# Kernel optimization log

Measured on AMD Instinct MI355X. Metric: run time of the kernel, lower is better.

The kernel has to match this reference:

```python
import jax, jax.numpy as jnp
import numpy as np

HEADS = 16
DIM_HEAD = 64
CHUNK = 64
EPS_LN = 1e-5
EPS_T5 = 1e-6


def _layernorm(x, g, b):
    mu = x.mean(-1, keepdims=True)
    var = x.var(-1, keepdims=True)
    return (x - mu) / jnp.sqrt(var + EPS_LN) * g + b


def _t5norm(x, w):
    # T5LayerNorm variant: divide by (||x|| * d^-0.5), i.e. RMS norm
    norm = jnp.linalg.norm(x, axis=-1, keepdims=True) * (x.shape[-1] ** -0.5)
    return x / jnp.maximum(norm, EPS_T5) * w


def _rotary(t, freqs):
    rot = freqs.shape[-1]
    t1, t2 = t[..., :rot], t[..., rot:]
    half = rot // 2
    a, b = t1[..., :half], t1[..., half:]
    rh = jnp.concatenate((-b, a), axis=-1)  # rotate_half
    t1 = t1 * jnp.cos(freqs) + rh * jnp.sin(freqs)
    return jnp.concatenate((t1, t2), axis=-1)


def _split_heads(t):
    B, N, _ = t.shape
    return t.reshape(B, N, HEADS, DIM_HEAD).transpose(0, 2, 1, 3)


def _merge_heads(t):
    B, H, N, D = t.shape
    return t.transpose(0, 2, 1, 3).reshape(B, N, H * D)


def _attend(q, k, v, causal=False):
    sim = jnp.einsum('bhid,bhjd->bhij', q, k)
    if causal:
        i, j = sim.shape[-2:]
        m = jnp.triu(jnp.ones((i, j), bool), j - i + 1)
        sim = jnp.where(m, jnp.finfo(sim.dtype).min, sim)
    attn = jax.nn.softmax(sim, axis=-1)
    return jnp.einsum('bhij,bhjd->bhid', attn, v)


def setup_inputs() -> dict:
    key = jax.random.key(0)
    ks = jax.random.split(key, 20)
    b, n, d = 4, 1024, 1024
    kc, r, rn = n // CHUNK, 2, 2 * CHUNK
    dff = 4 * d
    s = 0.02

    def W(i, *shape):
        return jax.random.normal(ks[i], shape, jnp.float32) * s

    return {
        'hidden_states': jax.random.normal(ks[0], (b, n, d), jnp.float32),
        'retrieval': jax.random.normal(ks[1], (b, kc, r, rn, d), jnp.float32),
        'q_pos_emb': jax.random.normal(ks[2], (1, 1, CHUNK, DIM_HEAD), jnp.float32),
        'k_pos_emb': jax.random.normal(ks[3], (1, 1, rn, DIM_HEAD), jnp.float32),
        'ln1_g': jnp.ones(d), 'ln1_b': jnp.zeros(d),
        'Wq_s': W(4, d, d), 'Wk_s': W(5, d, d), 'Wv_s': W(6, d, d),
        'Wo_s': W(7, d, d), 'bo_s': jnp.zeros(d),
        'ln2_g': jnp.ones(d), 'ln2_b': jnp.zeros(d),
        'Wq_c': W(8, d, d), 'Wk_c': W(9, d, d), 'Wv_c': W(10, d, d),
        'Wo_c': W(11, d, d), 'bo_c': jnp.zeros(d),
        'null_k': jax.random.normal(ks[12], (d,), jnp.float32),
        'null_v': jax.random.normal(ks[13], (d,), jnp.float32),
        'post_w': jnp.ones(d),
        'W1': W(14, d, dff), 'b1': jnp.zeros(dff),
        'W2': W(15, dff, d), 'b2': jnp.zeros(d),
    }


def reference(hidden_states, retrieval, q_pos_emb, k_pos_emb,
              ln1_g, ln1_b, Wq_s, Wk_s, Wv_s, Wo_s, bo_s,
              ln2_g, ln2_b, Wq_c, Wk_c, Wv_c, Wo_c, bo_c,
              null_k, null_v, post_w, W1, b1, W2, b2):
    b, n, d = hidden_states.shape
    scale = DIM_HEAD ** -0.5

    # --- causal self-attention (pre-LN) ---
    x = _layernorm(hidden_states, ln1_g, ln1_b)
    q = _split_heads(x @ Wq_s) * scale
    k = _split_heads(x @ Wk_s)
    v = _split_heads(x @ Wv_s)
    o = _merge_heads(_attend(q, k, v, causal=True)) @ Wo_s + bo_s
    hs = _layernorm(o + hidden_states, ln2_g, ln2_b)
    residual = hs  # residual taken after ln_2, before cross-attn (per source)

    # --- chunked cross-attention over retrieved neighbor chunks ---
    kc, r, rn = retrieval.shape[1:4]
    cp = CHUNK - 1  # causal padding
    seq_index = (n // CHUNK) * CHUNK
    # shift queries back by chunk_size-1 (causality), pad tail with zeros
    xq = jnp.pad(hs[:, cp:], ((0, 0), (0, cp), (0, 0)))[:, :seq_index]
    xq = xq.reshape(b * kc, CHUNK, d)
    ctx = retrieval.reshape(b * kc, r * rn, d)
    qpe = jnp.pad(q_pos_emb[:, :, cp:], ((0, 0), (0, 0), (0, cp), (0, 0)))
    kpe = jnp.tile(k_pos_emb, (1, 1, r, 1))  # 'b h n d -> b h (r n) d'
    q = _rotary(_split_heads(xq @ Wq_c) * scale, qpe)
    kk = _rotary(_split_heads(ctx @ Wk_c), kpe)
    vv = _split_heads(ctx @ Wv_c)
    nk = jnp.broadcast_to(null_k.reshape(1, HEADS, 1, DIM_HEAD), (b * kc, HEADS, 1, DIM_HEAD))
    nv = jnp.broadcast_to(null_v.reshape(1, HEADS, 1, DIM_HEAD), (b * kc, HEADS, 1, DIM_HEAD))
    kk = jnp.concatenate((nk, kk), axis=2)
    vv = jnp.concatenate((nv, vv), axis=2)
    cca = _merge_heads(_attend(q, kk, vv)) @ Wo_c + bo_c
    cca = cca.reshape(b, seq_index, d)
    # shift output forward by chunk_size-1, crop to n
    cca = jnp.pad(cca, ((0, 0), (cp, 0), (0, 0)))[:, :n]
    # PostNorm wrapper: T5 norm of (fn(x) + x)
    hs = _t5norm(cca + hs, post_w)

    # --- GPTNeo MLP (gelu-new / tanh approx) ---
    ff = jax.nn.gelu(hs @ W1 + b1, approximate=True) @ W2 + b2
    return residual + ff
```

## Files before the change

kernel.cpp:

```cpp
#include <hip/hip_runtime.h>
#include <hip/hip_bf16.h>
#include <math.h>

using u16 = unsigned short;

static constexpr int SEQ = 1024;
static constexpr int DM  = 1024;
static constexpr int DHD = 64;

typedef __bf16 bfv8 __attribute__((ext_vector_type(8)));
typedef float  f32x4 __attribute__((ext_vector_type(4)));

__device__ __forceinline__ float u2f(u16 u) {
  return __uint_as_float(((unsigned int)u) << 16);
}
__device__ __forceinline__ u16 f2b(float x) {
  __hip_bfloat16 h = __float2bfloat16(x);
  return *reinterpret_cast<u16*>(&h);
}
__device__ __forceinline__ void gload16(const u16* g, u16* l) {
  __builtin_amdgcn_global_load_lds(
      (const __attribute__((address_space(1))) unsigned int*)g,
      (__attribute__((address_space(3))) unsigned int*)l, 16, 0, 0);
}

template <int OT , bool HASBIAS, bool HASRES, bool DOGELU, bool ROT, int DBUF>
__global__ __launch_bounds__(256) void mgemm_k(
    const u16* __restrict__ A, const u16* __restrict__ Bt, void* __restrict__ C,
    int M, int K, int ldc, int coff, float alpha0, float alpha1, int acol,
    const float* __restrict__ bias, const float* __restrict__ res,
    const float* __restrict__ tab) {
  constexpr int NBUF = DBUF ? 2 : 1;
  __shared__ u16 As[NBUF][128 * 64];
  __shared__ u16 Bs[NBUF][128 * 64];
  const int tid = threadIdx.x;
  const int w = tid >> 6, lane = tid & 63;
  const int wr = w >> 1, wc = w & 1;

  const int nwg = gridDim.x * gridDim.y;
  const int bid = blockIdx.y * gridDim.x + blockIdx.x;
  const int qq = nwg >> 3, r8 = nwg & 7;
  const int xcd = bid & 7, pos = bid >> 3;
  const int cbase = (xcd < r8) ? xcd * (qq + 1) : r8 * (qq + 1) + (xcd - r8) * qq;
  const int logical = cbase + pos;
  const int row0 = (logical / gridDim.x) << 7;
  const int col0 = (logical % gridDim.x) << 7;

  f32x4 acc[4][4] = {};

  auto STAGE = [&](int buf, int k0) {
#pragma unroll
    for (int i = 0; i < 4; ++i) {
      const int c = ((w << 2) + i) * 64 + lane;
      const int r = c >> 3;
      const int cbs = ((c & 7) ^ (r & 7)) << 3;
      const int r64 = r & 63;
      const int rB = (r & 64) | ((r64 & 15) << 2) | (r64 >> 4);
      gload16(A + (size_t)(row0 + r) * K + k0 + cbs, &As[buf][((w << 2) + i) << 9]);
      gload16(Bt + (size_t)(col0 + rB) * K + k0 + cbs, &Bs[buf][((w << 2) + i) << 9]);
    }
  };
  auto COMPUTE = [&](int buf) {
#pragma unroll
    for (int kk = 0; kk < 2; ++kk) {
      bfv8 af[4], bfr[4];
#pragma unroll
      for (int m = 0; m < 4; ++m) {
        const int ar = (wr << 6) + (m << 4) + (lane & 15);
        const int sl = ((kk << 2) | (lane >> 4)) ^ (ar & 7);
        af[m] = *reinterpret_cast<const bfv8*>(&As[buf][ar * 64 + (sl << 3)]);
      }
#pragma unroll
      for (int n = 0; n < 4; ++n) {
        const int br = (wc << 6) + (n << 4) + (lane & 15);
        const int sl = ((kk << 2) | (lane >> 4)) ^ (br & 7);
        bfr[n] = *reinterpret_cast<const bfv8*>(&Bs[buf][br * 64 + (sl << 3)]);
      }
#pragma unroll
      for (int m = 0; m < 4; ++m)
#pragma unroll
        for (int n = 0; n < 4; ++n)
          acc[m][n] = __builtin_amdgcn_mfma_f32_16x16x32_bf16(af[m], bfr[n], acc[m][n], 0, 0, 0);
    }
  };

  if constexpr (DBUF) {
    STAGE(0, 0);
    int cur = 0;
    for (int k0 = 0; k0 < K; k0 += 64) {
      if (k0 + 64 < K) {
        STAGE(cur ^ 1, k0 + 64);
        asm volatile("s_waitcnt vmcnt(8)" ::: "memory");
      } else {
        asm volatile("s_waitcnt vmcnt(0)" ::: "memory");
      }
      __builtin_amdgcn_s_barrier();
      __builtin_amdgcn_sched_barrier(0);
      COMPUTE(cur);
      __builtin_amdgcn_s_barrier();
      cur ^= 1;
    }
  } else {
    for (int k0 = 0; k0 < K; k0 += 64) {
      STAGE(0, k0);
      __syncthreads();
      COMPUTE(0);
      __syncthreads();
    }
  }

  const int lr = (lane >> 4) << 2;
  const int lc = lane & 15;
  const int gcb = col0 + (wc << 6) + (lc << 2);
#pragma unroll
  for (int m = 0; m < 4; ++m) {
#pragma unroll
    for (int r = 0; r < 4; ++r) {
      const int gr = row0 + (wr << 6) + (m << 4) + lr + r;
      float t[4];
#pragma unroll
      for (int n = 0; n < 4; ++n)
        t[n] = acc[m][n][r] * ((gcb + n) < acol ? alpha0 : alpha1);
      if constexpr (ROT) {
        const int j = gr & 127;
        const int cc = gcb & 63;
        float4 c4 = *reinterpret_cast<const float4*>(tab + j * 64 + cc);
        float4 s4 = *reinterpret_cast<const float4*>(tab + 8192 + j * 64 + cc);
        const float cs[4] = {c4.x, c4.y, c4.z, c4.w};
        const float sn[4] = {s4.x, s4.y, s4.z, s4.w};
        float o2[4];
#pragma unroll
        for (int n = 0; n < 4; ++n) {
          const float pv = __shfl_xor(t[n], 8);
          const float part = (cc < 32) ? -pv : pv;
          o2[n] = t[n] * cs[n] + part * sn[n];
        }
#pragma unroll
        for (int n = 0; n < 4; ++n) t[n] = o2[n];
      }
      if constexpr (HASBIAS) {
        float4 b4 = *reinterpret_cast<const float4*>(bias + gcb);
        t[0] += b4.x; t[1] += b4.y; t[2] += b4.z; t[3] += b4.w;
      }
      if constexpr (DOGELU) {
#pragma unroll
        for (int n = 0; n < 4; ++n) {
          const float x = t[n];
          t[n] = 0.5f * x * (1.f + tanhf(0.7978845608f * (x + 0.044715f * x * x * x)));
        }
      }
      const size_t cb = (size_t)gr * ldc + coff + gcb;
      if constexpr (HASRES) {
        float4 r4 = *reinterpret_cast<const float4*>(res + cb);
        t[0] += r4.x; t[1] += r4.y; t[2] += r4.z; t[3] += r4.w;
      }
      if constexpr (OT == 0) {
        float4 o4 = make_float4(t[0], t[1], t[2], t[3]);
        *reinterpret_cast<float4*>((float*)C + cb) = o4;
      } else {
        ushort4 o4 = {f2b(t[0]), f2b(t[1]), f2b(t[2]), f2b(t[3])};
        *reinterpret_cast<ushort4*>((u16*)C + cb) = o4;
      }
    }
  }
}

__global__ __launch_bounds__(256) void costab_k(const float* __restrict__ kpe,
                                                float* __restrict__ tab) {
  const int i = blockIdx.x * 256 + threadIdx.x;
  const float f = kpe[i];
  tab[i] = cosf(f);
  tab[8192 + i] = sinf(f);
}

__global__ __launch_bounds__(256) void wtrans_k(const float* __restrict__ in,
                                                u16* __restrict__ out, int K, int N) {
  __shared__ float t[32][33];
  const int tx = threadIdx.x & 31, ty = threadIdx.x >> 5;
  const int r0 = blockIdx.y << 5, c0 = blockIdx.x << 5;
#pragma unroll
  for (int i = 0; i < 4; ++i)
    t[ty + 8 * i][tx] = in[(size_t)(r0 + ty + 8 * i) * N + c0 + tx];
  __syncthreads();
#pragma unroll
  for (int i = 0; i < 4; ++i)
    out[(size_t)(c0 + ty + 8 * i) * K + r0 + tx] = f2b(t[tx][ty + 8 * i]);
}

__global__ __launch_bounds__(256) void cast_k(const float* __restrict__ in,
                                              u16* __restrict__ out) {
  const int i = blockIdx.x * 256 + threadIdx.x;
  float4 v = reinterpret_cast<const float4*>(in)[i];
  ushort4 o = {f2b(v.x), f2b(v.y), f2b(v.z), f2b(v.w)};
  reinterpret_cast<ushort4*>(out)[i] = o;
}

__global__ __launch_bounds__(256) void ln_k(const float* __restrict__ in,
                                            const float* __restrict__ g,
                                            const float* __restrict__ b,
                                            u16* __restrict__ out) {
  const int tid = threadIdx.x;
  const int c = tid << 2;
  const size_t base = (size_t)blockIdx.x * DM;
  float4 x = *reinterpret_cast<const float4*>(in + base + c);
  float s = x.x + x.y + x.z + x.w;
  float ss = x.x * x.x + x.y * x.y + x.z * x.z + x.w * x.w;
#pragma unroll
  for (int m = 1; m < 64; m <<= 1) {
    s += __shfl_xor(s, m, 64);
    ss += __shfl_xor(ss, m, 64);
  }
  __shared__ float ls[4], lss[4];
  if ((tid & 63) == 0) { ls[tid >> 6] = s; lss[tid >> 6] = ss; }
  __syncthreads();
  s = (ls[0] + ls[1]) + (ls[2] + ls[3]);
  ss = (lss[0] + lss[1]) + (lss[2] + lss[3]);
  const float mu = s * (1.f / DM);
  const float var = ss * (1.f / DM) - mu * mu;
  const float rstd = rsqrtf(var + 1e-5f);
  float4 g4 = *reinterpret_cast<const float4*>(g + c);
  float4 b4 = *reinterpret_cast<const float4*>(b + c);
  ushort4 u;
  u.x = f2b((x.x - mu) * rstd * g4.x + b4.x);
  u.y = f2b((x.y - mu) * rstd * g4.y + b4.y);
  u.z = f2b((x.z - mu) * rstd * g4.z + b4.z);
  u.w = f2b((x.w - mu) * rstd * g4.w + b4.w);
  *reinterpret_cast<ushort4*>(out + base + c) = u;
}

__global__ __launch_bounds__(256) void ln2x_k(const float* __restrict__ in,
                                              const float* __restrict__ g,
                                              const float* __restrict__ b,
                                              float* __restrict__ hs,
                                              u16* __restrict__ xq) {
  const int tid = threadIdx.x;
  const int c = tid << 2;
  const int row = blockIdx.x;
  const size_t base = (size_t)row * DM;
  float4 x = *reinterpret_cast<const float4*>(in + base + c);
  float s = x.x + x.y + x.z + x.w;
  float ss = x.x * x.x + x.y * x.y + x.z * x.z + x.w * x.w;
#pragma unroll
  for (int m = 1; m < 64; m <<= 1) {
    s += __shfl_xor(s, m, 64);
    ss += __shfl_xor(ss, m, 64);
  }
  __shared__ float ls[4], lss[4];
  if ((tid & 63) == 0) { ls[tid >> 6] = s; lss[tid >> 6] = ss; }
  __syncthreads();
  s = (ls[0] + ls[1]) + (ls[2] + ls[3]);
  ss = (lss[0] + lss[1]) + (lss[2] + lss[3]);
  const float mu = s * (1.f / DM);
  const float var = ss * (1.f / DM) - mu * mu;
  const float rstd = rsqrtf(var + 1e-5f);
  float4 g4 = *reinterpret_cast<const float4*>(g + c);
  float4 b4 = *reinterpret_cast<const float4*>(b + c);
  float4 o;
  o.x = (x.x - mu) * rstd * g4.x + b4.x;
  o.y = (x.y - mu) * rstd * g4.y + b4.y;
  o.z = (x.z - mu) * rstd * g4.z + b4.z;
  o.w = (x.w - mu) * rstd * g4.w + b4.w;
  *reinterpret_cast<float4*>(hs + base + c) = o;
  const int local = row & (SEQ - 1);
  const int bb = row >> 10;
  if (local >= 63) {
    ushort4 u = {f2b(o.x), f2b(o.y), f2b(o.z), f2b(o.w)};
    *reinterpret_cast<ushort4*>(xq + (size_t)((bb << 10) + local - 63) * DM + c) = u;
  } else {
    ushort4 z = {0, 0, 0, 0};
    *reinterpret_cast<ushort4*>(xq + (size_t)((bb << 10) + 961 + local) * DM + c) = z;
  }
}

__global__ __launch_bounds__(256) void t5_k(const u16* __restrict__ cca,
                                            const float* __restrict__ hs,
                                            const float* __restrict__ w,
                                            u16* __restrict__ out) {
  const int tid = threadIdx.x;
  const int row = blockIdx.x;
  const int t = row & (SEQ - 1);
  const int c = tid << 2;
  const size_t base = (size_t)row * DM;
  float4 x = *reinterpret_cast<const float4*>(hs + base + c);
  if (t >= 63) {
    ushort4 cu = *reinterpret_cast<const ushort4*>(cca + base - (size_t)63 * DM + c);
    x.x += u2f(cu.x); x.y += u2f(cu.y); x.z += u2f(cu.z); x.w += u2f(cu.w);
  }
  float ss = x.x * x.x + x.y * x.y + x.z * x.z + x.w * x.w;
#pragma unroll
  for (int m = 1; m < 64; m <<= 1) ss += __shfl_xor(ss, m, 64);
  __shared__ float lss[4];
  if ((tid & 63) == 0) lss[tid >> 6] = ss;
  __syncthreads();
  ss = (lss[0] + lss[1]) + (lss[2] + lss[3]);
  const float rms = sqrtf(ss * (1.f / DM));
  const float inv = 1.f / fmaxf(rms, 1e-6f);
  float4 w4 = *reinterpret_cast<const float4*>(w + c);
  ushort4 o = {f2b(x.x * inv * w4.x), f2b(x.y * inv * w4.y),
               f2b(x.z * inv * w4.z), f2b(x.w * inv * w4.w)};
  *reinterpret_cast<ushort4*>(out + base + c) = o;
}

__global__ __launch_bounds__(256) void rotq_k(u16* __restrict__ q,
                                              const float* __restrict__ qpe) {
  __shared__ float rb[DM];
  const size_t base = (size_t)blockIdx.x * 64 * DM;
  const int e = threadIdx.x << 2;
  ushort4 u = *reinterpret_cast<const ushort4*>(q + base + e);
  rb[e + 0] = u2f(u.x); rb[e + 1] = u2f(u.y); rb[e + 2] = u2f(u.z); rb[e + 3] = u2f(u.w);
  __syncthreads();
  u16 ov[4];
#pragma unroll
  for (int k = 0; k < 4; ++k) {
    const int ee = e + k;
    const int cc = ee & 63;
    const float f = qpe[63 * 64 + cc];
    const float t1 = rb[ee];
    const float part = (cc < 32) ? -rb[ee + 32] : rb[ee - 32];
    ov[k] = f2b(t1 * cosf(f) + part * sinf(f));
  }
  ushort4 o = {ov[0], ov[1], ov[2], ov[3]};
  *reinterpret_cast<ushort4*>(q + base + e) = o;
}

__device__ __forceinline__ int vswz(int d, int k) {
  return (k & 7) | (((k >> 3) ^ ((d >> 2) & 7)) << 3);
}

__global__ __launch_bounds__(256) void attn_self_k(const u16* __restrict__ qkv,
                                                   u16* __restrict__ o) {
  const int qt = blockIdx.x, h = blockIdx.y, b = blockIdx.z;
  __shared__ u16 qs[64][72];
  __shared__ u16 ks[64][72];
  __shared__ u16 vt[64][72];
  __shared__ u16 ps[64][72];
  const int tid = threadIdx.x;
  const int w = tid >> 6, lane = tid & 63;
  const int strip = w << 4;
  const int lrow = lane & 15, lk = lane >> 4;
  const int rowb = b * SEQ;
  const int hoff = h * DHD;

#pragma unroll
  for (int rp = 0; rp < 4; ++rp) {
    const int fi = tid + (rp << 8);
    const int r = fi >> 4, c4 = (fi & 15) << 2;
    *reinterpret_cast<ushort4*>(&qs[r][c4]) =
        *reinterpret_cast<const ushort4*>(qkv + (size_t)(rowb + qt * 64 + r) * 3072 + hoff + c4);
  }

  ushort4 kr[4], vr[4];
  auto loadKV = [&](int kt) {
#pragma unroll
    for (int rp = 0; rp < 4; ++rp) {
      const int fi = tid + (rp << 8);
      const int r = fi >> 4, c4 = (fi & 15) << 2;
      const size_t g = (size_t)(rowb + kt * 64 + r) * 3072 + hoff + c4;
      kr[rp] = *reinterpret_cast<const ushort4*>(qkv + g + 1024);
      vr[rp] = *reinterpret_cast<const ushort4*>(qkv + g + 2048);
    }
  };
  loadKV(0);

  float mrun[4], lrun[4];
  f32x4 accO[4] = {};
#pragma unroll
  for (int r = 0; r < 4; ++r) { mrun[r] = -1e30f; lrun[r] = 0.f; }

  for (int kt = 0; kt <= qt; ++kt) {
    __syncthreads();
#pragma unroll
    for (int rp = 0; rp < 4; ++rp) {
      const int fi = tid + (rp << 8);
      const int r = fi >> 4, c4 = (fi & 15) << 2;
      *reinterpret_cast<ushort4*>(&ks[r][c4]) = kr[rp];
      vt[c4 + 0][vswz(c4 + 0, r)] = vr[rp].x;
      vt[c4 + 1][vswz(c4 + 1, r)] = vr[rp].y;
      vt[c4 + 2][vswz(c4 + 2, r)] = vr[rp].z;
      vt[c4 + 3][vswz(c4 + 3, r)] = vr[rp].w;
    }
    __syncthreads();
    if (kt < qt) loadKV(kt + 1);

    f32x4 sacc[4] = {};
#pragma unroll
    for (int kk = 0; kk < 2; ++kk) {
      bfv8 qf = *reinterpret_cast<const bfv8*>(&qs[strip + lrow][(kk << 5) + (lk << 3)]);
#pragma unroll
      for (int n = 0; n < 4; ++n) {
        bfv8 kf = *reinterpret_cast<const bfv8*>(&ks[(n << 4) + lrow][(kk << 5) + (lk << 3)]);
        sacc[n] = __builtin_amdgcn_mfma_f32_16x16x32_bf16(qf, kf, sacc[n], 0, 0, 0);
      }
    }
    if (kt == qt) {
#pragma unroll
      for (int n = 0; n < 4; ++n)
#pragma unroll
        for (int r = 0; r < 4; ++r)
          if ((n << 4) + lrow > strip + (lk << 2) + r) sacc[n][r] = -1e30f;
    }
#pragma unroll
    for (int r = 0; r < 4; ++r) {
      float mt = fmaxf(fmaxf(sacc[0][r], sacc[1][r]), fmaxf(sacc[2][r], sacc[3][r]));
      mt = fmaxf(mt, __shfl_xor(mt, 1));
      mt = fmaxf(mt, __shfl_xor(mt, 2));
      mt = fmaxf(mt, __shfl_xor(mt, 4));
      mt = fmaxf(mt, __shfl_xor(mt, 8));
      const float nm = fmaxf(mrun[r], mt);
      const float f = __expf(mrun[r] - nm);
      mrun[r] = nm;
      float p0 = __expf(sacc[0][r] - nm);
      float p1 = __expf(sacc[1][r] - nm);
      float p2 = __expf(sacc[2][r] - nm);
      float p3 = __expf(sacc[3][r] - nm);
      float rs = (p0 + p1) + (p2 + p3);
      rs += __shfl_xor(rs, 1);
      rs += __shfl_xor(rs, 2);
      rs += __shfl_xor(rs, 4);
      rs += __shfl_xor(rs, 8);
      lrun[r] = lrun[r] * f + rs;
#pragma unroll
      for (int nd = 0; nd < 4; ++nd) accO[nd][r] *= f;
      const int prow = strip + (lk << 2) + r;
      ps[prow][lrow +  0] = f2b(p0);
      ps[prow][lrow + 16] = f2b(p1);
      ps[prow][lrow + 32] = f2b(p2);
      ps[prow][lrow + 48] = f2b(p3);
    }
#pragma unroll
    for (int kk = 0; kk < 2; ++kk) {
      bfv8 pf = *reinterpret_cast<const bfv8*>(&ps[strip + lrow][(kk << 5) + (lk << 3)]);
#pragma unroll
      for (int nd = 0; nd < 4; ++nd) {
        const int vd = (nd << 4) + lrow;
        const int slot = ((kk << 2) | lk) ^ ((vd >> 2) & 7);
        bfv8 vf = *reinterpret_cast<const bfv8*>(&vt[vd][slot << 3]);
        accO[nd] = __builtin_amdgcn_mfma_f32_16x16x32_bf16(pf, vf, accO[nd], 0, 0, 0);
      }
    }
  }
#pragma unroll
  for (int r = 0; r < 4; ++r) {
    const float inv = 1.f / lrun[r];
    const size_t rowoff = (size_t)(rowb + qt * 64 + strip + (lk << 2) + r) * DM + hoff;
#pragma unroll
    for (int nd = 0; nd < 4; ++nd)
      o[rowoff + (nd << 4) + lrow] = f2b(accO[nd][r] * inv);
  }
}

__global__ __launch_bounds__(256) void attn_cca_k(
    const u16* __restrict__ q, const u16* __restrict__ kv,
    const float* __restrict__ nullk, const float* __restrict__ nullv,
    u16* __restrict__ o) {
  const int h = blockIdx.y, bk = blockIdx.z;
  __shared__ u16 qs[64][72];
  __shared__ u16 ks[64][72];
  __shared__ u16 vt[64][72];
  __shared__ u16 ps[64][72];
  const int tid = threadIdx.x;
  const int w = tid >> 6, lane = tid & 63;
  const int strip = w << 4;
  const int lrow = lane & 15, lk = lane >> 4;
  const int hoff = h * DHD;
  const size_t qbase = (size_t)bk * 64 * DM + hoff;

#pragma unroll
  for (int rp = 0; rp < 4; ++rp) {
    const int fi = tid + (rp << 8);
    const int r = fi >> 4, c4 = (fi & 15) << 2;
    *reinterpret_cast<ushort4*>(&qs[r][c4]) =
        *reinterpret_cast<const ushort4*>(q + qbase + (size_t)r * DM + c4);
  }

  ushort4 kr[4], vr[4];
  auto loadKV = [&](int kt) {
#pragma unroll
    for (int rp = 0; rp < 4; ++rp) {
      const int fi = tid + (rp << 8);
      const int r = fi >> 4, c4 = (fi & 15) << 2;
      const int kj = kt * 64 + r;
      ushort4 ku = {0, 0, 0, 0}, vu = {0, 0, 0, 0};
      if (kj == 0) {
        float4 nk4 = *reinterpret_cast<const float4*>(nullk + hoff + c4);
        float4 nv4 = *reinterpret_cast<const float4*>(nullv + hoff + c4);
        ku = {f2b(nk4.x), f2b(nk4.y), f2b(nk4.z), f2b(nk4.w)};
        vu = {f2b(nv4.x), f2b(nv4.y), f2b(nv4.z), f2b(nv4.w)};
      } else if (kj <= 256) {
        const size_t g = (size_t)(bk * 256 + kj - 1) * 2048 + hoff + c4;
        ku = *reinterpret_cast<const ushort4*>(kv + g);
        vu = *reinterpret_cast<const ushort4*>(kv + g + 1024);
      }
      kr[rp] = ku; vr[rp] = vu;
    }
  };
  loadKV(0);

  float mrun[4], lrun[4];
  f32x4 accO[4] = {};
#pragma unroll
  for (int r = 0; r < 4; ++r) { mrun[r] = -1e30f; lrun[r] = 0.f; }

  for (int kt = 0; kt < 5; ++kt) {
    __syncthreads();
#pragma unroll
    for (int rp = 0; rp < 4; ++rp) {
      const int fi = tid + (rp << 8);
      const int r = fi >> 4, c4 = (fi & 15) << 2;
      *reinterpret_cast<ushort4*>(&ks[r][c4]) = kr[rp];
      vt[c4 + 0][vswz(c4 + 0, r)] = vr[rp].x;
      vt[c4 + 1][vswz(c4 + 1, r)] = vr[rp].y;
      vt[c4 + 2][vswz(c4 + 2, r)] = vr[rp].z;
      vt[c4 + 3][vswz(c4 + 3, r)] = vr[rp].w;
    }
    __syncthreads();
    if (kt < 4) loadKV(kt + 1);

    f32x4 sacc[4] = {};
#pragma unroll
    for (int kk = 0; kk < 2; ++kk) {
      bfv8 qf = *reinterpret_cast<const bfv8*>(&qs[strip + lrow][(kk << 5) + (lk << 3)]);
#pragma unroll
      for (int n = 0; n < 4; ++n) {
        bfv8 kf = *reinterpret_cast<const bfv8*>(&ks[(n << 4) + lrow][(kk << 5) + (lk << 3)]);
        sacc[n] = __builtin_amdgcn_mfma_f32_16x16x32_bf16(qf, kf, sacc[n], 0, 0, 0);
      }
    }
    if (kt == 4) {
#pragma unroll
      for (int n = 0; n < 4; ++n)
#pragma unroll
        for (int r = 0; r < 4; ++r)
          if ((n << 4) + lrow >= 1) sacc[n][r] = -1e30f;
    }
#pragma unroll
    for (int r = 0; r < 4; ++r) {
      float mt = fmaxf(fmaxf(sacc[0][r], sacc[1][r]), fmaxf(sacc[2][r], sacc[3][r]));
      mt = fmaxf(mt, __shfl_xor(mt, 1));
      mt = fmaxf(mt, __shfl_xor(mt, 2));
      mt = fmaxf(mt, __shfl_xor(mt, 4));
      mt = fmaxf(mt, __shfl_xor(mt, 8));
      const float nm = fmaxf(mrun[r], mt);
      const float f = __expf(mrun[r] - nm);
      mrun[r] = nm;
      float p0 = __expf(sacc[0][r] - nm);
      float p1 = __expf(sacc[1][r] - nm);
      float p2 = __expf(sacc[2][r] - nm);
      float p3 = __expf(sacc[3][r] - nm);
      float rs = (p0 + p1) + (p2 + p3);
      rs += __shfl_xor(rs, 1);
      rs += __shfl_xor(rs, 2);
      rs += __shfl_xor(rs, 4);
      rs += __shfl_xor(rs, 8);
      lrun[r] = lrun[r] * f + rs;
#pragma unroll
      for (int nd = 0; nd < 4; ++nd) accO[nd][r] *= f;
      const int prow = strip + (lk << 2) + r;
      ps[prow][lrow +  0] = f2b(p0);
      ps[prow][lrow + 16] = f2b(p1);
      ps[prow][lrow + 32] = f2b(p2);
      ps[prow][lrow + 48] = f2b(p3);
    }
#pragma unroll
    for (int kk = 0; kk < 2; ++kk) {
      bfv8 pf = *reinterpret_cast<const bfv8*>(&ps[strip + lrow][(kk << 5) + (lk << 3)]);
#pragma unroll
      for (int nd = 0; nd < 4; ++nd) {
        const int vd = (nd << 4) + lrow;
        const int slot = ((kk << 2) | lk) ^ ((vd >> 2) & 7);
        bfv8 vf = *reinterpret_cast<const bfv8*>(&vt[vd][slot << 3]);
        accO[nd] = __builtin_amdgcn_mfma_f32_16x16x32_bf16(pf, vf, accO[nd], 0, 0, 0);
      }
    }
  }
#pragma unroll
  for (int r = 0; r < 4; ++r) {
    const float inv = 1.f / lrun[r];
    const size_t rowoff = (size_t)(bk * 64 + strip + (lk << 2) + r) * DM + hoff;
#pragma unroll
    for (int nd = 0; nd < 4; ++nd)
      o[rowoff + (nd << 4) + lrow] = f2b(accO[nd][r] * inv);
  }
}

extern "C" void kernel_launch(void* const* d_in, const int* in_sizes, int n_in,
                              void* d_out, int out_size, void* d_ws, size_t ws_size,
                              hipStream_t stream) {
  const float* hidden    = (const float*)d_in[0];
  const float* retrieval = (const float*)d_in[1];
  const float* q_pos     = (const float*)d_in[2];
  const float* k_pos     = (const float*)d_in[3];
  const float* ln1_g     = (const float*)d_in[4];
  const float* ln1_b     = (const float*)d_in[5];
  const float* Wq_s      = (const float*)d_in[6];
  const float* Wk_s      = (const float*)d_in[7];
  const float* Wv_s      = (const float*)d_in[8];
  const float* Wo_s      = (const float*)d_in[9];
  const float* bo_s      = (const float*)d_in[10];
  const float* ln2_g     = (const float*)d_in[11];
  const float* ln2_b     = (const float*)d_in[12];
  const float* Wq_c      = (const float*)d_in[13];
  const float* Wk_c      = (const float*)d_in[14];
  const float* Wv_c      = (const float*)d_in[15];
  const float* Wo_c      = (const float*)d_in[16];
  const float* bo_c      = (const float*)d_in[17];
  const float* null_k    = (const float*)d_in[18];
  const float* null_v    = (const float*)d_in[19];
  const float* post_w    = (const float*)d_in[20];
  const float* W1        = (const float*)d_in[21];
  const float* b1        = (const float*)d_in[22];
  const float* W2        = (const float*)d_in[23];
  const float* b2        = (const float*)d_in[24];
  float* out = (float*)d_out;

  constexpr size_t MB = 1024 * 1024;
  constexpr size_t ME = 1024 * 1024;
  char* W = (char*)d_ws;
  u16* Wt_qkv  = (u16*)(W + 0 * MB);
  u16* Wt_os   = (u16*)(W + 6 * MB);
  u16* Wt_qc   = (u16*)(W + 8 * MB);
  u16* Wt_kcvc = (u16*)(W + 10 * MB);
  u16* Wt_oc   = (u16*)(W + 14 * MB);
  u16* W1t     = (u16*)(W + 16 * MB);
  u16* W2t     = (u16*)(W + 24 * MB);
  float* s5    = (float*)(W + 32 * MB);
  float* s0    = (float*)(W + 48 * MB);
  u16* retb    = (u16*)(W + 48 * MB);
  u16* ccab    = (u16*)(W + 48 * MB);
  u16* ccapb   = (u16*)(W + 56 * MB);
  u16* xb      = (u16*)(W + 64 * MB);
  u16* t5b     = (u16*)(W + 64 * MB);
  u16* attnb   = (u16*)(W + 80 * MB);
  u16* xqb     = (u16*)(W + 80 * MB);
  float* tab   = (float*)(W + 80 * MB);
  u16* qkvb    = (u16*)(W + 88 * MB);
  u16* qcb     = (u16*)(W + 88 * MB);
  u16* kkvvb   = (u16*)(W + 96 * MB);
  u16* ff1b    = (u16*)(W + 96 * MB);

  const dim3 blk(256);

  wtrans_k<<<dim3(32, 32), blk, 0, stream>>>(Wq_s, Wt_qkv + 0 * ME, 1024, 1024);
  wtrans_k<<<dim3(32, 32), blk, 0, stream>>>(Wk_s, Wt_qkv + 1 * ME, 1024, 1024);
  wtrans_k<<<dim3(32, 32), blk, 0, stream>>>(Wv_s, Wt_qkv + 2 * ME, 1024, 1024);
  wtrans_k<<<dim3(32, 32), blk, 0, stream>>>(Wo_s, Wt_os, 1024, 1024);
  wtrans_k<<<dim3(32, 32), blk, 0, stream>>>(Wq_c, Wt_qc, 1024, 1024);
  wtrans_k<<<dim3(32, 32), blk, 0, stream>>>(Wk_c, Wt_kcvc + 0 * ME, 1024, 1024);
  wtrans_k<<<dim3(32, 32), blk, 0, stream>>>(Wv_c, Wt_kcvc + 1 * ME, 1024, 1024);
  wtrans_k<<<dim3(32, 32), blk, 0, stream>>>(Wo_c, Wt_oc, 1024, 1024);
  wtrans_k<<<dim3(128, 32), blk, 0, stream>>>(W1, W1t, 1024, 4096);
  wtrans_k<<<dim3(32, 128), blk, 0, stream>>>(W2, W2t, 4096, 1024);

  ln_k<<<dim3(4096), blk, 0, stream>>>(hidden, ln1_g, ln1_b, xb);
  mgemm_k<1, false, false, false, false, 1><<<dim3(24, 32), blk, 0, stream>>>(
      xb, Wt_qkv, qkvb, 4096, 1024, 3072, 0, 0.125f, 1.f, 1024, nullptr, nullptr, nullptr);
  attn_self_k<<<dim3(16, 16, 4), blk, 0, stream>>>(qkvb, attnb);
  mgemm_k<0, true, true, false, false, 1><<<dim3(8, 32), blk, 0, stream>>>(
      attnb, Wt_os, s0, 4096, 1024, 1024, 0, 1.f, 1.f, 0, bo_s, hidden, nullptr);
  ln2x_k<<<dim3(4096), blk, 0, stream>>>(s0, ln2_g, ln2_b, s5, xqb);
  cast_k<<<dim3(16384), blk, 0, stream>>>(retrieval, retb);
  mgemm_k<1, false, false, false, false, 1><<<dim3(8, 32), blk, 0, stream>>>(
      xqb, Wt_qc, qcb, 4096, 1024, 1024, 0, 1.f, 0.125f, 0, nullptr, nullptr, nullptr);
  rotq_k<<<dim3(64), blk, 0, stream>>>(qcb, q_pos);
  costab_k<<<dim3(32), blk, 0, stream>>>(k_pos, tab);
  mgemm_k<1, false, false, false, true, 0><<<dim3(8, 128), blk, 0, stream>>>(
      retb, Wt_kcvc, kkvvb, 16384, 1024, 2048, 0, 1.f, 1.f, 0, nullptr, nullptr, tab);
  mgemm_k<1, false, false, false, false, 0><<<dim3(8, 128), blk, 0, stream>>>(
      retb, Wt_kcvc + 1024 * 1024, kkvvb, 16384, 1024, 2048, 1024, 1.f, 1.f, 0,
      nullptr, nullptr, nullptr);
  attn_cca_k<<<dim3(1, 16, 64), blk, 0, stream>>>(qcb, kkvvb, null_k, null_v, ccab);
  mgemm_k<1, true, false, false, false, 1><<<dim3(8, 32), blk, 0, stream>>>(
      ccab, Wt_oc, ccapb, 4096, 1024, 1024, 0, 1.f, 1.f, 0, bo_c, nullptr, nullptr);
  t5_k<<<dim3(4096), blk, 0, stream>>>(ccapb, s5, post_w, t5b);
  mgemm_k<1, true, false, true, false, 0><<<dim3(32, 32), blk, 0, stream>>>(
      t5b, W1t, ff1b, 4096, 1024, 4096, 0, 1.f, 1.f, 0, b1, nullptr, nullptr);
  mgemm_k<0, true, true, false, false, 1><<<dim3(8, 32), blk, 0, stream>>>(
      ff1b, W2t, out, 4096, 4096, 1024, 0, 1.f, 1.f, 0, b2, s5, nullptr);
}
```

Baseline: 508.0 us.

## Split-K the FF2 GEMM and widen self-attention blocks to 128 query rows

The final 4096x1024x4096 GEMM is split along K into two partial products written to a scratch buffer. A new reduce kernel sums the partials and adds bias and residual, which doubles the workgroup count for a launch that previously had only 256 blocks. Self-attention now uses 512-thread blocks covering 128 query rows, so each K/V tile loaded into LDS is shared by twice as many warps, with per-warp causal skipping. The costs are extra fp32 partial traffic, one more kernel launch, and some idle warps in the upper half of each block.

```diff
diff --git a/kernel.cpp b/kernel.cpp
--- a/kernel.cpp
+++ b/kernel.cpp
@@ -24,10 +24,10 @@
       (__attribute__((address_space(3))) unsigned int*)l, 16, 0, 0);
 }
 
-template <int OT , bool HASBIAS, bool HASRES, bool DOGELU, bool ROT, int DBUF>
+template <int OT, bool HASBIAS, bool HASRES, bool DOGELU, bool ROT, int DBUF, int PART>
 __global__ __launch_bounds__(256) void mgemm_k(
     const u16* __restrict__ A, const u16* __restrict__ Bt, void* __restrict__ C,
-    int M, int K, int ldc, int coff, float alpha0, float alpha1, int acol,
+    int M, int K, int lda, int ldc, int coff, float alpha0, float alpha1, int acol,
     const float* __restrict__ bias, const float* __restrict__ res,
     const float* __restrict__ tab) {
   constexpr int NBUF = DBUF ? 2 : 1;
@@ -36,6 +36,7 @@
   const int tid = threadIdx.x;
   const int w = tid >> 6, lane = tid & 63;
   const int wr = w >> 1, wc = w & 1;
+  const int koff = blockIdx.z * K;
 
   const int nwg = gridDim.x * gridDim.y;
   const int bid = blockIdx.y * gridDim.x + blockIdx.x;
@@ -56,8 +57,8 @@
       const int cbs = ((c & 7) ^ (r & 7)) << 3;
       const int r64 = r & 63;
       const int rB = (r & 64) | ((r64 & 15) << 2) | (r64 >> 4);
-      gload16(A + (size_t)(row0 + r) * K + k0 + cbs, &As[buf][((w << 2) + i) << 9]);
-      gload16(Bt + (size_t)(col0 + rB) * K + k0 + cbs, &Bs[buf][((w << 2) + i) << 9]);
+      gload16(A + (size_t)(row0 + r) * lda + koff + k0 + cbs, &As[buf][((w << 2) + i) << 9]);
+      gload16(Bt + (size_t)(col0 + rB) * lda + koff + k0 + cbs, &Bs[buf][((w << 2) + i) << 9]);
     }
   };
   auto COMPUTE = [&](int buf) {
@@ -149,7 +150,8 @@
           t[n] = 0.5f * x * (1.f + tanhf(0.7978845608f * (x + 0.044715f * x * x * x)));
         }
       }
-      const size_t cb = (size_t)gr * ldc + coff + gcb;
+      size_t cb = (size_t)gr * ldc + coff + gcb;
+      if constexpr (PART) cb += (size_t)blockIdx.z * M * ldc;
       if constexpr (HASRES) {
         float4 r4 = *reinterpret_cast<const float4*>(res + cb);
         t[0] += r4.x; t[1] += r4.y; t[2] += r4.z; t[3] += r4.w;
@@ -163,6 +165,24 @@
       }
     }
   }
+}
+
+__global__ __launch_bounds__(256) void reduce_k(const float* __restrict__ p,
+                                                const float* __restrict__ bias,
+                                                const float* __restrict__ res,
+                                                float* __restrict__ out) {
+  const int i = blockIdx.x * 256 + threadIdx.x;
+  const int col = (i & 255) << 2;
+  float4 a = reinterpret_cast<const float4*>(p)[i];
+  float4 b = reinterpret_cast<const float4*>(p + (size_t)4096 * 1024)[i];
+  float4 b4 = *reinterpret_cast<const float4*>(bias + col);
+  float4 r4 = reinterpret_cast<const float4*>(res)[i];
+  float4 o;
+  o.x = a.x + b.x + b4.x + r4.x;
+  o.y = a.y + b.y + b4.y + r4.y;
+  o.z = a.z + b.z + b4.z + r4.z;
+  o.w = a.w + b.w + b4.w + r4.w;
+  reinterpret_cast<float4*>(out)[i] = o;
 }
 
 __global__ __launch_bounds__(256) void costab_k(const float* __restrict__ kpe,
@@ -327,33 +347,35 @@
   return (k & 7) | (((k >> 3) ^ ((d >> 2) & 7)) << 3);
 }
 
-__global__ __launch_bounds__(256) void attn_self_k(const u16* __restrict__ qkv,
+__global__ __launch_bounds__(512) void attn_self_k(const u16* __restrict__ qkv,
                                                    u16* __restrict__ o) {
   const int qt = blockIdx.x, h = blockIdx.y, b = blockIdx.z;
-  __shared__ u16 qs[64][72];
+  __shared__ u16 qs[128][72];
   __shared__ u16 ks[64][72];
   __shared__ u16 vt[64][72];
-  __shared__ u16 ps[64][72];
+  __shared__ u16 ps[128][72];
   const int tid = threadIdx.x;
   const int w = tid >> 6, lane = tid & 63;
   const int strip = w << 4;
+  const int sloc = (w & 3) << 4;
   const int lrow = lane & 15, lk = lane >> 4;
   const int rowb = b * SEQ;
   const int hoff = h * DHD;
+  const int qrow0 = qt << 7;
 
 #pragma unroll
   for (int rp = 0; rp < 4; ++rp) {
-    const int fi = tid + (rp << 8);
+    const int fi = tid + (rp << 9);
     const int r = fi >> 4, c4 = (fi & 15) << 2;
     *reinterpret_cast<ushort4*>(&qs[r][c4]) =
-        *reinterpret_cast<const ushort4*>(qkv + (size_t)(rowb + qt * 64 + r) * 3072 + hoff + c4);
-  }
-
-  ushort4 kr[4], vr[4];
+        *reinterpret_cast<const ushort4*>(qkv + (size_t)(rowb + qrow0 + r) * 3072 + hoff + c4);
+  }
+
+  ushort4 kr[2], vr[2];
   auto loadKV = [&](int kt) {
 #pragma unroll
-    for (int rp = 0; rp < 4; ++rp) {
-      const int fi = tid + (rp << 8);
+    for (int rp = 0; rp < 2; ++rp) {
+      const int fi = tid + (rp << 9);
       const int r = fi >> 4, c4 = (fi & 15) << 2;
       const size_t g = (size_t)(rowb + kt * 64 + r) * 3072 + hoff + c4;
       kr[rp] = *reinterpret_cast<const ushort4*>(qkv + g + 1024);
@@ -362,16 +384,19 @@
   };
   loadKV(0);
 
+  const int ktmax = 2 * qt + 1;
+  const int ktd = 2 * qt + (w >> 2);
+
   float mrun[4], lrun[4];
   f32x4 accO[4] = {};
 #pragma unroll
   for (int r = 0; r < 4; ++r) { mrun[r] = -1e30f; lrun[r] = 0.f; }
 
-  for (int kt = 0; kt <= qt; ++kt) {
+  for (int kt = 0; kt <= ktmax; ++kt) {
     __syncthreads();
 #pragma unroll
-    for (int rp = 0; rp < 4; ++rp) {
-      const int fi = tid + (rp << 8);
+    for (int rp = 0; rp < 2; ++rp) {
+      const int fi = tid + (rp << 9);
       const int r = fi >> 4, c4 = (fi & 15) << 2;
       *reinterpret_cast<ushort4*>(&ks[r][c4]) = kr[rp];
       vt[c4 + 0][vswz(c4 + 0, r)] = vr[rp].x;
@@ -380,69 +405,71 @@
       vt[c4 + 3][vswz(c4 + 3, r)] = vr[rp].w;
     }
     __syncthreads();
-    if (kt < qt) loadKV(kt + 1);
-
-    f32x4 sacc[4] = {};
-#pragma unroll
-    for (int kk = 0; kk < 2; ++kk) {
-      bfv8 qf = *reinterpret_cast<const bfv8*>(&qs[strip + lrow][(kk << 5) + (lk << 3)]);
-#pragma unroll
-      for (int n = 0; n < 4; ++n) {
-        bfv8 kf = *reinterpret_cast<const bfv8*>(&ks[(n << 4) + lrow][(kk << 5) + (lk << 3)]);
-        sacc[n] = __builtin_amdgcn_mfma_f32_16x16x32_bf16(qf, kf, sacc[n], 0, 0, 0);
-      }
-    }
-    if (kt == qt) {
-#pragma unroll
-      for (int n = 0; n < 4; ++n)
-#pragma unroll
-        for (int r = 0; r < 4; ++r)
-          if ((n << 4) + lrow > strip + (lk << 2) + r) sacc[n][r] = -1e30f;
-    }
-#pragma unroll
-    for (int r = 0; r < 4; ++r) {
-      float mt = fmaxf(fmaxf(sacc[0][r], sacc[1][r]), fmaxf(sacc[2][r], sacc[3][r]));
-      mt = fmaxf(mt, __shfl_xor(mt, 1));
-      mt = fmaxf(mt, __shfl_xor(mt, 2));
-      mt = fmaxf(mt, __shfl_xor(mt, 4));
-      mt = fmaxf(mt, __shfl_xor(mt, 8));
-      const float nm = fmaxf(mrun[r], mt);
-      const float f = __expf(mrun[r] - nm);
-      mrun[r] = nm;
-      float p0 = __expf(sacc[0][r] - nm);
-      float p1 = __expf(sacc[1][r] - nm);
-      float p2 = __expf(sacc[2][r] - nm);
-      float p3 = __expf(sacc[3][r] - nm);
-      float rs = (p0 + p1) + (p2 + p3);
-      rs += __shfl_xor(rs, 1);
-      rs += __shfl_xor(rs, 2);
-      rs += __shfl_xor(rs, 4);
-      rs += __shfl_xor(rs, 8);
-      lrun[r] = lrun[r] * f + rs;
-#pragma unroll
-      for (int nd = 0; nd < 4; ++nd) accO[nd][r] *= f;
-      const int prow = strip + (lk << 2) + r;
-      ps[prow][lrow +  0] = f2b(p0);
-      ps[prow][lrow + 16] = f2b(p1);
-      ps[prow][lrow + 32] = f2b(p2);
-      ps[prow][lrow + 48] = f2b(p3);
-    }
-#pragma unroll
-    for (int kk = 0; kk < 2; ++kk) {
-      bfv8 pf = *reinterpret_cast<const bfv8*>(&ps[strip + lrow][(kk << 5) + (lk << 3)]);
-#pragma unroll
-      for (int nd = 0; nd < 4; ++nd) {
-        const int vd = (nd << 4) + lrow;
-        const int slot = ((kk << 2) | lk) ^ ((vd >> 2) & 7);
-        bfv8 vf = *reinterpret_cast<const bfv8*>(&vt[vd][slot << 3]);
-        accO[nd] = __builtin_amdgcn_mfma_f32_16x16x32_bf16(pf, vf, accO[nd], 0, 0, 0);
+    if (kt < ktmax) loadKV(kt + 1);
+
+    if (kt <= ktd) {
+      f32x4 sacc[4] = {};
+#pragma unroll
+      for (int kk = 0; kk < 2; ++kk) {
+        bfv8 qf = *reinterpret_cast<const bfv8*>(&qs[strip + lrow][(kk << 5) + (lk << 3)]);
+#pragma unroll
+        for (int n = 0; n < 4; ++n) {
+          bfv8 kf = *reinterpret_cast<const bfv8*>(&ks[(n << 4) + lrow][(kk << 5) + (lk << 3)]);
+          sacc[n] = __builtin_amdgcn_mfma_f32_16x16x32_bf16(qf, kf, sacc[n], 0, 0, 0);
+        }
+      }
+      if (kt == ktd) {
+#pragma unroll
+        for (int n = 0; n < 4; ++n)
+#pragma unroll
+          for (int r = 0; r < 4; ++r)
+            if ((n << 4) + lrow > sloc + (lk << 2) + r) sacc[n][r] = -1e30f;
+      }
+#pragma unroll
+      for (int r = 0; r < 4; ++r) {
+        float mt = fmaxf(fmaxf(sacc[0][r], sacc[1][r]), fmaxf(sacc[2][r], sacc[3][r]));
+        mt = fmaxf(mt, __shfl_xor(mt, 1));
+        mt = fmaxf(mt, __shfl_xor(mt, 2));
+        mt = fmaxf(mt, __shfl_xor(mt, 4));
+        mt = fmaxf(mt, __shfl_xor(mt, 8));
+        const float nm = fmaxf(mrun[r], mt);
+        const float f = __expf(mrun[r] - nm);
+        mrun[r] = nm;
+        float p0 = __expf(sacc[0][r] - nm);
+        float p1 = __expf(sacc[1][r] - nm);
+        float p2 = __expf(sacc[2][r] - nm);
+        float p3 = __expf(sacc[3][r] - nm);
+        float rs = (p0 + p1) + (p2 + p3);
+        rs += __shfl_xor(rs, 1);
+        rs += __shfl_xor(rs, 2);
+        rs += __shfl_xor(rs, 4);
+        rs += __shfl_xor(rs, 8);
+        lrun[r] = lrun[r] * f + rs;
+#pragma unroll
+        for (int nd = 0; nd < 4; ++nd) accO[nd][r] *= f;
+        const int prow = strip + (lk << 2) + r;
+        ps[prow][lrow +  0] = f2b(p0);
+        ps[prow][lrow + 16] = f2b(p1);
+        ps[prow][lrow + 32] = f2b(p2);
+        ps[prow][lrow + 48] = f2b(p3);
+      }
+#pragma unroll
+      for (int kk = 0; kk < 2; ++kk) {
+        bfv8 pf = *reinterpret_cast<const bfv8*>(&ps[strip + lrow][(kk << 5) + (lk << 3)]);
+#pragma unroll
+        for (int nd = 0; nd < 4; ++nd) {
+          const int vd = (nd << 4) + lrow;
+          const int slot = ((kk << 2) | lk) ^ ((vd >> 2) & 7);
+          bfv8 vf = *reinterpret_cast<const bfv8*>(&vt[vd][slot << 3]);
+          accO[nd] = __builtin_amdgcn_mfma_f32_16x16x32_bf16(pf, vf, accO[nd], 0, 0, 0);
+        }
       }
     }
   }
 #pragma unroll
   for (int r = 0; r < 4; ++r) {
     const float inv = 1.f / lrun[r];
-    const size_t rowoff = (size_t)(rowb + qt * 64 + strip + (lk << 2) + r) * DM + hoff;
+    const size_t rowoff = (size_t)(rowb + qrow0 + strip + (lk << 2) + r) * DM + hoff;
 #pragma unroll
     for (int nd = 0; nd < 4; ++nd)
       o[rowoff + (nd << 4) + lrow] = f2b(accO[nd][r] * inv);
@@ -637,6 +664,7 @@
   u16* qcb     = (u16*)(W + 88 * MB);
   u16* kkvvb   = (u16*)(W + 96 * MB);
   u16* ff1b    = (u16*)(W + 96 * MB);
+  float* fpart = (float*)(W + 128 * MB);
 
   const dim3 blk(256);
 
@@ -652,28 +680,29 @@
   wtrans_k<<<dim3(32, 128), blk, 0, stream>>>(W2, W2t, 4096, 1024);
 
   ln_k<<<dim3(4096), blk, 0, stream>>>(hidden, ln1_g, ln1_b, xb);
-  mgemm_k<1, false, false, false, false, 1><<<dim3(24, 32), blk, 0, stream>>>(
-      xb, Wt_qkv, qkvb, 4096, 1024, 3072, 0, 0.125f, 1.f, 1024, nullptr, nullptr, nullptr);
-  attn_self_k<<<dim3(16, 16, 4), blk, 0, stream>>>(qkvb, attnb);
-  mgemm_k<0, true, true, false, false, 1><<<dim3(8, 32), blk, 0, stream>>>(
-      attnb, Wt_os, s0, 4096, 1024, 1024, 0, 1.f, 1.f, 0, bo_s, hidden, nullptr);
+  mgemm_k<1, false, false, false, false, 1, 0><<<dim3(24, 32), blk, 0, stream>>>(
+      xb, Wt_qkv, qkvb, 4096, 1024, 1024, 3072, 0, 0.125f, 1.f, 1024, nullptr, nullptr, nullptr);
+  attn_self_k<<<dim3(8, 16, 4), dim3(512), 0, stream>>>(qkvb, attnb);
+  mgemm_k<0, true, true, false, false, 1, 0><<<dim3(8, 32), blk, 0, stream>>>(
+      attnb, Wt_os, s0, 4096, 1024, 1024, 1024, 0, 1.f, 1.f, 0, bo_s, hidden, nullptr);
   ln2x_k<<<dim3(4096), blk, 0, stream>>>(s0, ln2_g, ln2_b, s5, xqb);
   cast_k<<<dim3(16384), blk, 0, stream>>>(retrieval, retb);
-  mgemm_k<1, false, false, false, false, 1><<<dim3(8, 32), blk, 0, stream>>>(
-      xqb, Wt_qc, qcb, 4096, 1024, 1024, 0, 1.f, 0.125f, 0, nullptr, nullptr, nullptr);
+  mgemm_k<1, false, false, false, false, 1, 0><<<dim3(8, 32), blk, 0, stream>>>(
+      xqb, Wt_qc, qcb, 4096, 1024, 1024, 1024, 0, 1.f, 0.125f, 0, nullptr, nullptr, nullptr);
   rotq_k<<<dim3(64), blk, 0, stream>>>(qcb, q_pos);
   costab_k<<<dim3(32), blk, 0, stream>>>(k_pos, tab);
-  mgemm_k<1, false, false, false, true, 0><<<dim3(8, 128), blk, 0, stream>>>(
-      retb, Wt_kcvc, kkvvb, 16384, 1024, 2048, 0, 1.f, 1.f, 0, nullptr, nullptr, tab);
-  mgemm_k<1, false, false, false, false, 0><<<dim3(8, 128), blk, 0, stream>>>(
-      retb, Wt_kcvc + 1024 * 1024, kkvvb, 16384, 1024, 2048, 1024, 1.f, 1.f, 0,
+  mgemm_k<1, false, false, false, true, 0, 0><<<dim3(8, 128), blk, 0, stream>>>(
+      retb, Wt_kcvc, kkvvb, 16384, 1024, 1024, 2048, 0, 1.f, 1.f, 0, nullptr, nullptr, tab);
+  mgemm_k<1, false, false, false, false, 0, 0><<<dim3(8, 128), blk, 0, stream>>>(
+      retb, Wt_kcvc + 1024 * 1024, kkvvb, 16384, 1024, 1024, 2048, 1024, 1.f, 1.f, 0,
       nullptr, nullptr, nullptr);
   attn_cca_k<<<dim3(1, 16, 64), blk, 0, stream>>>(qcb, kkvvb, null_k, null_v, ccab);
-  mgemm_k<1, true, false, false, false, 1><<<dim3(8, 32), blk, 0, stream>>>(
-      ccab, Wt_oc, ccapb, 4096, 1024, 1024, 0, 1.f, 1.f, 0, bo_c, nullptr, nullptr);
+  mgemm_k<1, true, false, false, false, 1, 0><<<dim3(8, 32), blk, 0, stream>>>(
+      ccab, Wt_oc, ccapb, 4096, 1024, 1024, 1024, 0, 1.f, 1.f, 0, bo_c, nullptr, nullptr);
   t5_k<<<dim3(4096), blk, 0, stream>>>(ccapb, s5, post_w, t5b);
-  mgemm_k<1, true, false, true, false, 0><<<dim3(32, 32), blk, 0, stream>>>(
-      t5b, W1t, ff1b, 4096, 1024, 4096, 0, 1.f, 1.f, 0, b1, nullptr, nullptr);
-  mgemm_k<0, true, true, false, false, 1><<<dim3(8, 32), blk, 0, stream>>>(
-      ff1b, W2t, out, 4096, 4096, 1024, 0, 1.f, 1.f, 0, b2, s5, nullptr);
-}
+  mgemm_k<1, true, false, true, false, 0, 0><<<dim3(32, 32), blk, 0, stream>>>(
+      t5b, W1t, ff1b, 4096, 1024, 1024, 4096, 0, 1.f, 1.f, 0, b1, nullptr, nullptr);
+  mgemm_k<0, false, false, false, false, 1, 1><<<dim3(8, 32, 2), blk, 0, stream>>>(
+      ff1b, W2t, fpart, 4096, 2048, 4096, 1024, 0, 1.f, 1.f, 0, nullptr, nullptr, nullptr);
+  reduce_k<<<dim3(4096), blk, 0, stream>>>(fpart, b2, s5, out);
+}
```

Measured after the change: 481.7 us. -5.2%, faster.
